# Optimization experiments

Hardware: AMD Instinct MI355X
Metric: run time of the kernel (lower is better)

Reference implementation:

```python
import jax, jax.numpy as jnp
import numpy as np

B, S, D_IN, D_OUT = 8, 4096, 1024, 1024
R_F, R_M, R_S = 8, 32, 64
R_TOT = R_F + R_M + R_S  # 104
HID = 64
ALPHA = 1.0


def setup_inputs() -> dict:
    key = jax.random.key(0)
    ks = jax.random.split(key, 10)
    inp = {
        "x": jax.random.normal(ks[0], (B, S, D_IN), dtype=jnp.float32),
        # fresh memory state after reset_memory(): zeros of shape [batch, r_*]
        "mem_fast": jnp.zeros((B, R_F), dtype=jnp.float32),
        "mem_medium": jnp.zeros((B, R_M), dtype=jnp.float32),
        "mem_slow": jnp.zeros((B, R_S), dtype=jnp.float32),
        # frozen base nn.Linear
        "base_w": jax.random.normal(ks[1], (D_OUT, D_IN), dtype=jnp.float32) / np.sqrt(D_IN),
        "base_b": jax.random.normal(ks[2], (D_OUT,), dtype=jnp.float32) * 0.01,
        # LoRA projections: proj_down kaiming-ish, proj_up zero-init per _init_weights
        "pd_w": jax.random.normal(ks[3], (R_TOT, D_IN), dtype=jnp.float32) / np.sqrt(D_IN),
        "pu_w": jax.random.normal(ks[4], (D_OUT, R_TOT), dtype=jnp.float32) * 0.01,
        # gate_net: Linear(D_IN, HID) -> GELU -> Linear(HID, 3) -> Softmax
        "g1_w": jax.random.normal(ks[5], (HID, D_IN), dtype=jnp.float32) / np.sqrt(D_IN),
        "g1_b": jnp.zeros((HID,), dtype=jnp.float32),
        "g2_w": jax.random.normal(ks[6], (3, HID), dtype=jnp.float32) / np.sqrt(HID),
        "g2_b": jnp.zeros((3,), dtype=jnp.float32),
    }
    return inp


def reference(x, mem_fast, mem_medium, mem_slow, base_w, base_b,
              pd_w, pu_w, g1_w, g1_b, g2_w, g2_b):
    # base linear: [B,S,D_out]
    base_out = jnp.einsum("bsd,od->bso", x, base_w) + base_b
    # down projection: [B,S,R_TOT]
    proj = jnp.einsum("bsd,rd->bsr", x, pd_w)
    # per-timescale multiplicative modulation by recurrent memory state
    # (split -> (1+mem)*proj -> concat) == concat memories once
    mem = jnp.concatenate([mem_fast, mem_medium, mem_slow], axis=-1)  # [B,R_TOT]
    modulated = proj * (1.0 + mem[:, None, :])
    # gate_net: Linear -> GELU(exact) -> Linear -> softmax over 3 timescales
    h = jax.nn.gelu(jnp.einsum("bsd,hd->bsh", x, g1_w) + g1_b, approximate=False)
    gates = jax.nn.softmax(jnp.einsum("bsh,gh->bsg", h, g2_w) + g2_b, axis=-1)
    gate_scale = jnp.mean(gates, axis=-1, keepdims=True)  # [B,S,1]
    # up projection and residual combine
    lora_out = jnp.einsum("bsr,or->bso", modulated, pu_w)
    output = base_out + ALPHA * lora_out * gate_scale
    return output
```

## Files before the change

kernel.cpp:

```cpp
#include <hip/hip_runtime.h>
#include <stdint.h>


typedef unsigned short ushort_t;
typedef unsigned short us8 __attribute__((ext_vector_type(8)));
typedef short short8 __attribute__((ext_vector_type(8)));
typedef float f32x4 __attribute__((ext_vector_type(4)));

__device__ __forceinline__ ushort_t f2b(float f) {
  union { float f; uint32_t i; } v; v.f = f;
  uint32_t lsb = (v.i >> 16) & 1u;
  v.i += 0x7fffu + lsb;
  return (ushort_t)(v.i >> 16);
}

__device__ __forceinline__ void async16(const void* g, void* l) {
  __builtin_amdgcn_global_load_lds(
      (const __attribute__((address_space(1))) void*)g,
      (__attribute__((address_space(3))) void*)l, 16, 0, 0);
}

__global__ __launch_bounds__(256) void convert_x(const float* __restrict__ x,
                                                 ushort_t* __restrict__ xb) {
  const int flat = blockIdx.x;
  const int b = flat & 7;
  const int c = flat >> 3;
  const size_t i = (((size_t)b * 2048 + c) * 256 + threadIdx.x) * 8;
  f32x4 a0 = *(const f32x4*)(x + i);
  f32x4 a1 = *(const f32x4*)(x + i + 4);
  us8 o;
#pragma unroll
  for (int j = 0; j < 4; j++) { o[j] = f2b(a0[j]); o[4 + j] = f2b(a1[j]); }
  *(us8*)(xb + i) = o;
}

__global__ __launch_bounds__(128) void prep(const float* __restrict__ base_w,
                                            const float* __restrict__ pu_w,
                                            const float* __restrict__ pd_w,
                                            const float* __restrict__ mf,
                                            const float* __restrict__ mm,
                                            const float* __restrict__ ms,
                                            ushort_t* __restrict__ W0,
                                            ushort_t* __restrict__ Weff,
                                            int* __restrict__ flags) {
  const int o = blockIdx.x, y = blockIdx.y, t = threadIdx.x;
  __shared__ float spu[104];
  __shared__ int sflag;
  ushort_t* dst;

  if (y == 0) {
    if (t < 104) spu[t] = pu_w[o * 104 + t] * (1.0f / 3.0f);
    dst = W0 + o * 1024;
    __syncthreads();
  } else {
    const int b = y - 1;
    if (t == 0) sflag = 0;
    __syncthreads();
    float mv = 0.0f;
    if (t < 104) {
      mv = (t < 8) ? mf[b * 8 + t]
         : (t < 40) ? mm[b * 32 + (t - 8)]
                    : ms[b * 64 + (t - 40)];
      if (mv != 0.0f) sflag = 1;
      spu[t] = pu_w[o * 104 + t] * (1.0f + mv) * (1.0f / 3.0f);
    }
    __syncthreads();
    if (o == 0 && t == 0) flags[b] = sflag;
    if (!sflag) return;
    dst = Weff + ((size_t)b << 20) + o * 1024;
  }

  const int d0 = t * 8;
  float acc[8];
  f32x4 b0 = *(const f32x4*)(base_w + o * 1024 + d0);
  f32x4 b1 = *(const f32x4*)(base_w + o * 1024 + d0 + 4);
#pragma unroll
  for (int j = 0; j < 4; j++) { acc[j] = b0[j]; acc[4 + j] = b1[j]; }
  for (int r = 0; r < 104; r++) {
    f32x4 p0 = *(const f32x4*)(pd_w + r * 1024 + d0);
    f32x4 p1 = *(const f32x4*)(pd_w + r * 1024 + d0 + 4);
    float s = spu[r];
#pragma unroll
    for (int j = 0; j < 4; j++) { acc[j] += s * p0[j]; acc[4 + j] += s * p1[j]; }
  }
  us8 ov;
#pragma unroll
  for (int j = 0; j < 8; j++) ov[j] = f2b(acc[j]);
  *(us8*)(dst + d0) = ov;
}

__global__ __launch_bounds__(512, 2) void gemm256(
    const ushort_t* __restrict__ xb, const float* __restrict__ base_b,
    const ushort_t* __restrict__ W0, const ushort_t* __restrict__ Weff,
    const int* __restrict__ flags, float* __restrict__ out) {
  const int flat = blockIdx.x;
  const int b  = flat & 7;
  const int i  = flat >> 3;
  const int bm = i >> 2;
  const int bn = i & 3;

  const ushort_t* W = flags[b] ? (Weff + ((size_t)b << 20)) : W0;

  __shared__ __align__(16) char lds[4 * 32768];

  const int t = threadIdx.x;
  const int w = t >> 6, l = t & 63;
  const int wr = w >> 2, wc = w & 3;
  const int row16 = l & 15, quad = l >> 4;

  const int srow = w * 16 + (l >> 2);
  const int scol = (((l & 3) ^ ((l >> 3) & 3))) * 8;
  const ushort_t* gA = xb + (((size_t)b * 4096 + bm * 256 + srow) << 10) + scol;
  const ushort_t* gB = W + (((size_t)(bn * 256 + srow)) << 10) + scol;

  const int qsw = (quad ^ ((row16 >> 1) & 3)) * 16;
  const int aoff = (wr * 128 + row16) * 64 + qsw;
  const int boff = 16384 + (wc * 64 + row16) * 64 + qsw;

#define STAGE_A(kt)                                                       \
  {                                                                       \
    const ushort_t* g_ = gA + (kt) * 32;                                  \
    char* d_ = lds + ((kt) & 3) * 32768 + w * 1024;                       \
    async16(g_, d_);                                                      \
    async16(g_ + (128 << 10), d_ + 8192);                                 \
  }
#define STAGE_B(kt)                                                       \
  {                                                                       \
    const ushort_t* g_ = gB + (kt) * 32;                                  \
    char* d_ = lds + ((kt) & 3) * 32768 + 16384 + w * 1024;               \
    async16(g_, d_);                                                      \
    async16(g_ + (128 << 10), d_ + 8192);                                 \
  }

  f32x4 acc[8][4] = {};

  STAGE_A(0) STAGE_B(0) STAGE_A(1) STAGE_B(1)
  asm volatile("s_waitcnt vmcnt(4)" ::: "memory");
  __builtin_amdgcn_s_barrier();

  for (int kt = 0; kt < 32; ++kt) {
    const char* cur = lds + (kt & 3) * 32768;

    short8 af[4], bf[4];
#pragma unroll
    for (int mi = 0; mi < 4; ++mi)
      af[mi] = *(const short8*)(cur + aoff + mi * 1024);
#pragma unroll
    for (int ni = 0; ni < 4; ++ni)
      bf[ni] = *(const short8*)(cur + boff + ni * 1024);
    if (kt < 30) STAGE_A(kt + 2)
    __builtin_amdgcn_sched_barrier(0);
    __builtin_amdgcn_s_barrier();
    __builtin_amdgcn_s_setprio(1);
#pragma unroll
    for (int mi = 0; mi < 4; ++mi)
#pragma unroll
      for (int ni = 0; ni < 4; ++ni)
        acc[mi][ni] = __builtin_amdgcn_mfma_f32_16x16x32_bf16(af[mi], bf[ni],
                                                              acc[mi][ni], 0, 0, 0);
    __builtin_amdgcn_s_setprio(0);

    short8 af2[4];
#pragma unroll
    for (int mi = 0; mi < 4; ++mi)
      af2[mi] = *(const short8*)(cur + aoff + (4 + mi) * 1024);
    if (kt < 30) STAGE_B(kt + 2)
    __builtin_amdgcn_sched_barrier(0);
    __builtin_amdgcn_s_barrier();
    __builtin_amdgcn_s_setprio(1);
#pragma unroll
    for (int mi = 0; mi < 4; ++mi)
#pragma unroll
      for (int ni = 0; ni < 4; ++ni)
        acc[4 + mi][ni] = __builtin_amdgcn_mfma_f32_16x16x32_bf16(af2[mi], bf[ni],
                                                                  acc[4 + mi][ni], 0, 0, 0);
    __builtin_amdgcn_s_setprio(0);

    if (kt < 30) {
      asm volatile("s_waitcnt vmcnt(4)" ::: "memory");
    } else if (kt == 30) {
      asm volatile("s_waitcnt vmcnt(0)" ::: "memory");
    }
    __builtin_amdgcn_s_barrier();
  }

#pragma unroll
  for (int ni = 0; ni < 4; ++ni) {
    const int col = bn * 256 + wc * 64 + ni * 16 + row16;
    const float bb = base_b[col];
#pragma unroll
    for (int mi = 0; mi < 8; ++mi) {
      const int row = bm * 256 + wr * 128 + mi * 16 + quad * 4;
      float* po = out + (((size_t)b * 4096 + row) << 10) + col;
#pragma unroll
      for (int i2 = 0; i2 < 4; ++i2)
        po[(size_t)i2 << 10] = acc[mi][ni][i2] + bb;
    }
  }
#undef STAGE_A
#undef STAGE_B
}

extern "C" void kernel_launch(void* const* d_in, const int* in_sizes, int n_in,
                              void* d_out, int out_size, void* d_ws, size_t ws_size,
                              hipStream_t stream) {
  const float* x  = (const float*)d_in[0];
  const float* mf = (const float*)d_in[1];
  const float* mm = (const float*)d_in[2];
  const float* ms = (const float*)d_in[3];
  const float* base_w = (const float*)d_in[4];
  const float* base_b = (const float*)d_in[5];
  const float* pd_w = (const float*)d_in[6];
  const float* pu_w = (const float*)d_in[7];

  char* ws = (char*)d_ws;
  int* flags     = (int*)ws;
  ushort_t* W0   = (ushort_t*)(ws + 4096);
  ushort_t* xb   = (ushort_t*)(ws + 4096 + (2u << 20));
  ushort_t* Weff = (ushort_t*)(ws + 4096 + (2u << 20) + (64u << 20));

  prep<<<dim3(1024, 9), 128, 0, stream>>>(base_w, pu_w, pd_w, mf, mm, ms,
                                          W0, Weff, flags);
  convert_x<<<16384, 256, 0, stream>>>(x, xb);
  gemm256<<<512, 512, 0, stream>>>(xb, base_b, W0, Weff, flags, (float*)d_out);
}
```

Baseline: 344.2 us.

## Fuse fp32-to-bf16 conversion of x into GEMM A-tile loading

```diff
diff --git a/kernel.cpp b/kernel.cpp
--- a/kernel.cpp
+++ b/kernel.cpp
@@ -18,20 +18,6 @@
   __builtin_amdgcn_global_load_lds(
       (const __attribute__((address_space(1))) void*)g,
       (__attribute__((address_space(3))) void*)l, 16, 0, 0);
-}
-
-__global__ __launch_bounds__(256) void convert_x(const float* __restrict__ x,
-                                                 ushort_t* __restrict__ xb) {
-  const int flat = blockIdx.x;
-  const int b = flat & 7;
-  const int c = flat >> 3;
-  const size_t i = (((size_t)b * 2048 + c) * 256 + threadIdx.x) * 8;
-  f32x4 a0 = *(const f32x4*)(x + i);
-  f32x4 a1 = *(const f32x4*)(x + i + 4);
-  us8 o;
-#pragma unroll
-  for (int j = 0; j < 4; j++) { o[j] = f2b(a0[j]); o[4 + j] = f2b(a1[j]); }
-  *(us8*)(xb + i) = o;
 }
 
 __global__ __launch_bounds__(128) void prep(const float* __restrict__ base_w,
@@ -90,7 +76,7 @@
 }
 
 __global__ __launch_bounds__(512, 2) void gemm256(
-    const ushort_t* __restrict__ xb, const float* __restrict__ base_b,
+    const float* __restrict__ x, const float* __restrict__ base_b,
     const ushort_t* __restrict__ W0, const ushort_t* __restrict__ Weff,
     const int* __restrict__ flags, float* __restrict__ out) {
   const int flat = blockIdx.x;
@@ -109,21 +95,20 @@
   const int row16 = l & 15, quad = l >> 4;
 
   const int srow = w * 16 + (l >> 2);
-  const int scol = (((l & 3) ^ ((l >> 3) & 3))) * 8;
-  const ushort_t* gA = xb + (((size_t)b * 4096 + bm * 256 + srow) << 10) + scol;
+  const int scol = ((l & 3) ^ ((l >> 3) & 3)) * 8;
   const ushort_t* gB = W + (((size_t)(bn * 256 + srow)) << 10) + scol;
+
+  const int ar = t >> 1;
+  const int ac = (t & 1) * 16;
+  const float* gA = x + (((size_t)b * 4096 + bm * 256 + ar) << 10) + ac;
+  const int fr_ = (ar >> 1) & 3;
+  const int ws0 = (((t & 1) * 2 + 0) ^ fr_) * 16;
+  const int ws1 = (((t & 1) * 2 + 1) ^ fr_) * 16;
 
   const int qsw = (quad ^ ((row16 >> 1) & 3)) * 16;
   const int aoff = (wr * 128 + row16) * 64 + qsw;
   const int boff = 16384 + (wc * 64 + row16) * 64 + qsw;
 
-#define STAGE_A(kt)                                                       \
-  {                                                                       \
-    const ushort_t* g_ = gA + (kt) * 32;                                  \
-    char* d_ = lds + ((kt) & 3) * 32768 + w * 1024;                       \
-    async16(g_, d_);                                                      \
-    async16(g_ + (128 << 10), d_ + 8192);                                 \
-  }
 #define STAGE_B(kt)                                                       \
   {                                                                       \
     const ushort_t* g_ = gB + (kt) * 32;                                  \
@@ -131,11 +116,32 @@
     async16(g_, d_);                                                      \
     async16(g_ + (128 << 10), d_ + 8192);                                 \
   }
+#define A_ISSUE(kt2)                                                      \
+  {                                                                       \
+    const float* p_ = gA + (kt2) * 32;                                    \
+    s0 = *(const f32x4*)(p_);      s1 = *(const f32x4*)(p_ + 4);          \
+    s2 = *(const f32x4*)(p_ + 8);  s3 = *(const f32x4*)(p_ + 12);         \
+  }
+#define A_WRITE(kt2)                                                      \
+  {                                                                       \
+    us8 o0, o1;                                                           \
+    _Pragma("unroll")                                                     \
+    for (int j_ = 0; j_ < 4; ++j_) {                                      \
+      o0[j_] = f2b(s0[j_]); o0[4 + j_] = f2b(s1[j_]);                     \
+      o1[j_] = f2b(s2[j_]); o1[4 + j_] = f2b(s3[j_]);                     \
+    }                                                                     \
+    char* d_ = lds + ((kt2) & 3) * 32768 + ar * 64;                       \
+    *(us8*)(d_ + ws0) = o0;                                               \
+    *(us8*)(d_ + ws1) = o1;                                               \
+  }
 
   f32x4 acc[8][4] = {};
-
-  STAGE_A(0) STAGE_B(0) STAGE_A(1) STAGE_B(1)
-  asm volatile("s_waitcnt vmcnt(4)" ::: "memory");
+  f32x4 s0, s1, s2, s3;
+
+  A_ISSUE(0) A_WRITE(0)
+  A_ISSUE(1) STAGE_B(0)
+  A_WRITE(1) STAGE_B(1)
+  asm volatile("s_waitcnt vmcnt(2) lgkmcnt(0)" ::: "memory");
   __builtin_amdgcn_s_barrier();
 
   for (int kt = 0; kt < 32; ++kt) {
@@ -148,7 +154,7 @@
 #pragma unroll
     for (int ni = 0; ni < 4; ++ni)
       bf[ni] = *(const short8*)(cur + boff + ni * 1024);
-    if (kt < 30) STAGE_A(kt + 2)
+    if (kt < 30) A_ISSUE(kt + 2)
     __builtin_amdgcn_sched_barrier(0);
     __builtin_amdgcn_s_barrier();
     __builtin_amdgcn_s_setprio(1);
@@ -164,7 +170,7 @@
 #pragma unroll
     for (int mi = 0; mi < 4; ++mi)
       af2[mi] = *(const short8*)(cur + aoff + (4 + mi) * 1024);
-    if (kt < 30) STAGE_B(kt + 2)
+    if (kt < 30) { STAGE_B(kt + 2) A_WRITE(kt + 2) }
     __builtin_amdgcn_sched_barrier(0);
     __builtin_amdgcn_s_barrier();
     __builtin_amdgcn_s_setprio(1);
@@ -176,11 +182,9 @@
                                                                   acc[4 + mi][ni], 0, 0, 0);
     __builtin_amdgcn_s_setprio(0);
 
-    if (kt < 30) {
-      asm volatile("s_waitcnt vmcnt(4)" ::: "memory");
-    } else if (kt == 30) {
-      asm volatile("s_waitcnt vmcnt(0)" ::: "memory");
-    }
+    if (kt == 30) asm volatile("s_waitcnt vmcnt(0)" ::: "memory");
+    asm volatile("s_waitcnt lgkmcnt(0)" ::: "memory");
+    __builtin_amdgcn_sched_barrier(0);
     __builtin_amdgcn_s_barrier();
   }
 
@@ -197,8 +201,9 @@
         po[(size_t)i2 << 10] = acc[mi][ni][i2] + bb;
     }
   }
-#undef STAGE_A
 #undef STAGE_B
+#undef A_ISSUE
+#undef A_WRITE
 }
 
 extern "C" void kernel_launch(void* const* d_in, const int* in_sizes, int n_in,
@@ -216,11 +221,9 @@
   char* ws = (char*)d_ws;
   int* flags     = (int*)ws;
   ushort_t* W0   = (ushort_t*)(ws + 4096);
-  ushort_t* xb   = (ushort_t*)(ws + 4096 + (2u << 20));
-  ushort_t* Weff = (ushort_t*)(ws + 4096 + (2u << 20) + (64u << 20));
+  ushort_t* Weff = (ushort_t*)(ws + 4096 + (2u << 20));
 
   prep<<<dim3(1024, 9), 128, 0, stream>>>(base_w, pu_w, pd_w, mf, mm, ms,
                                           W0, Weff, flags);
-  convert_x<<<16384, 256, 0, stream>>>(x, xb);
-  gemm256<<<512, 512, 0, stream>>>(xb, base_b, W0, Weff, flags, (float*)d_out);
-}
+  gemm256<<<512, 512, 0, stream>>>(x, base_b, W0, Weff, flags, (float*)d_out);
+}
```

New measurement: 351.8 us. +2.2%, slower.
